# Kernel optimization log

Measured on AMD Instinct MI355X. Metric: run time of the kernel, lower is better.

Reference implementation:

```python
import jax, jax.numpy as jnp
import numpy as np

N, M, FIN, FOUT, K = 16, 65536, 32, 32, 7


def setup_inputs() -> dict:
    key = jax.random.key(0)
    k1, k2, k3, k4, k5 = jax.random.split(key, 5)
    stdv = 1.0 / np.sqrt(FIN)
    x = jax.random.normal(k1, (N, M, FIN), dtype=jnp.float32)
    weight = jax.random.uniform(k2, (K, FIN, FOUT), dtype=jnp.float32, minval=-stdv, maxval=stdv)
    bias = jax.random.uniform(k3, (FOUT,), dtype=jnp.float32, minval=-stdv, maxval=stdv)
    index_list = jax.random.randint(k4, (M * K,), 0, M, dtype=jnp.int32)
    index_value = jax.random.uniform(k5, (M, K), dtype=jnp.float32)
    return {"x": x, "weight": weight, "bias": bias,
            "index_list": index_list, "index_value": index_value}


def reference(x, weight, bias, index_list, index_value):
    # out[n,m,o] = sum_k sum_f index_value[m,k] * x[n, idx[m,k], f] * weight[k,f,o] + bias[o]
    n, m, fin = x.shape
    k = index_value.shape[1]
    idx = index_list.reshape(m, k)            # [M, K] neighbor ids
    gathered = x[:, idx, :]                    # [N, M, K, Fin] gather of neighbor feats
    weighted = gathered * index_value[None, :, :, None]  # apply adjacency weights
    out = jnp.einsum('nmkf,kfo->nmo', weighted, weight) + bias
    return out
```

## Files before the change

kernel.cpp:

```cpp
#include <hip/hip_runtime.h>
#include <hip/hip_bf16.h>

#define N_    16
#define M_    65536
#define FIN_  32
#define FOUT_ 32
#define K_    7

typedef __bf16 bf16x8 __attribute__((ext_vector_type(8)));
typedef float  f32x4  __attribute__((ext_vector_type(4)));

__global__ __launch_bounds__(256, 4)
void gfc_kernel(const float* __restrict__ x,
                const float* __restrict__ w,
                const float* __restrict__ bias,
                const int*   __restrict__ index_list,
                const float* __restrict__ index_value,
                float* __restrict__ out)
{
    const int lane  = threadIdx.x & 63;
    const int col   = lane & 15;
    const int kgrp  = lane >> 4;

    const int waves_per_block = blockDim.x >> 6;
    const int wave_id     = blockIdx.x * waves_per_block + (threadIdx.x >> 6);
    const int total_waves = gridDim.x * waves_per_block;

    bf16x8 bfrag[K_][2];
    #pragma unroll
    for (int k = 0; k < K_; ++k) {
        #pragma unroll
        for (int h = 0; h < 2; ++h) {
            const float* wp = w + (size_t)k * (FIN_ * FOUT_)
                                + (size_t)(kgrp * 8) * FOUT_ + h * 16 + col;
            bf16x8 b;
            #pragma unroll
            for (int j = 0; j < 8; ++j)
                b[j] = (__bf16)wp[j * FOUT_];
            bfrag[k][h] = b;
        }
    }
    const float b_lo = bias[col];
    const float b_hi = bias[16 + col];

    for (int m = wave_id; m < M_; m += total_waves) {
        f32x4 acc0 = {0.f, 0.f, 0.f, 0.f};
        f32x4 acc1 = {0.f, 0.f, 0.f, 0.f};

        #pragma unroll
        for (int k = 0; k < K_; ++k) {
            const int   m2  = index_list[m * K_ + k];
            const float ivk = index_value[m * K_ + k];

            const float* ap = x + ((size_t)col * M_ + (size_t)m2) * FIN_ + kgrp * 8;
            const float4 v0 = *(const float4*)(ap);
            const float4 v1 = *(const float4*)(ap + 4);

            const float av[8] = {v0.x, v0.y, v0.z, v0.w, v1.x, v1.y, v1.z, v1.w};
            bf16x8 a;
            #pragma unroll
            for (int j = 0; j < 8; ++j)
                a[j] = (__bf16)(av[j] * ivk);

            acc0 = __builtin_amdgcn_mfma_f32_16x16x32_bf16(a, bfrag[k][0], acc0, 0, 0, 0);
            acc1 = __builtin_amdgcn_mfma_f32_16x16x32_bf16(a, bfrag[k][1], acc1, 0, 0, 0);
        }

        #pragma unroll
        for (int r = 0; r < 4; ++r) {
            const int n = kgrp * 4 + r;
            const size_t base = ((size_t)n * M_ + (size_t)m) * FOUT_;
            out[base + col]      = acc0[r] + b_lo;
            out[base + 16 + col] = acc1[r] + b_hi;
        }
    }
}

extern "C" void kernel_launch(void* const* d_in, const int* in_sizes, int n_in,
                              void* d_out, int out_size, void* d_ws, size_t ws_size,
                              hipStream_t stream) {
    const float* x    = (const float*)d_in[0];
    const float* w    = (const float*)d_in[1];
    const float* bias = (const float*)d_in[2];
    const int*   il   = (const int*)  d_in[3];
    const float* iv   = (const float*)d_in[4];
    float* out = (float*)d_out;

    dim3 grid(2048), block(256);
    hipLaunchKernelGGL(gfc_kernel, grid, block, 0, stream, x, w, bias, il, iv, out);
}
```

Before: 363.5 us.

## Pre-transpose x to bf16 [M,N,F] layout for contiguous neighbor gathers

Adds a pre-pass that converts x to bf16 and lays it out as [M][N][FIN], so each gathered neighbor row of 16 batches by 32 features is one contiguous 1 KB block instead of 16 scattered 128-byte pieces. The main kernel loads all K indices and neighbor fragments up front to overlap memory latency, and uses readfirstlane to keep the row index scalar. The cost is an extra full pass over x (read fp32, write bf16) plus a workspace buffer. It also adds an extra rounding step, since x is rounded to bf16 before the index-value scale is applied. A fallback to the old kernel is kept for when the workspace is too small.

```diff
diff --git a/kernel.cpp b/kernel.cpp
--- a/kernel.cpp
+++ b/kernel.cpp
@@ -10,13 +10,108 @@
 typedef __bf16 bf16x8 __attribute__((ext_vector_type(8)));
 typedef float  f32x4  __attribute__((ext_vector_type(4)));
 
+__global__ __launch_bounds__(256)
+void transpose_kernel(const float* __restrict__ x, __bf16* __restrict__ xT)
+{
+    const int tid = blockIdx.x * blockDim.x + threadIdx.x;
+    const int f8 = tid & 3;
+    const int n  = (tid >> 2) & 15;
+    const int m  = tid >> 6;
+
+    const float4* src = (const float4*)(x + ((size_t)n * M_ + m) * FIN_ + f8 * 8);
+    const float4 v0 = src[0];
+    const float4 v1 = src[1];
+    const float av[8] = {v0.x, v0.y, v0.z, v0.w, v1.x, v1.y, v1.z, v1.w};
+
+    bf16x8 b;
+    #pragma unroll
+    for (int j = 0; j < 8; ++j) b[j] = (__bf16)av[j];
+
+    *(bf16x8*)(xT + ((size_t)m * N_ + n) * FIN_ + f8 * 8) = b;
+}
+
 __global__ __launch_bounds__(256, 4)
-void gfc_kernel(const float* __restrict__ x,
-                const float* __restrict__ w,
-                const float* __restrict__ bias,
-                const int*   __restrict__ index_list,
-                const float* __restrict__ index_value,
-                float* __restrict__ out)
+void gfc_bf16_kernel(const __bf16* __restrict__ xT,
+                     const float* __restrict__ w,
+                     const float* __restrict__ bias,
+                     const int*   __restrict__ index_list,
+                     const float* __restrict__ index_value,
+                     float* __restrict__ out)
+{
+    const int lane  = threadIdx.x & 63;
+    const int col   = lane & 15;
+    const int kgrp  = lane >> 4;
+
+    const int waves_per_block = blockDim.x >> 6;
+    const int wave_id     = blockIdx.x * waves_per_block + (threadIdx.x >> 6);
+    const int total_waves = gridDim.x * waves_per_block;
+
+    bf16x8 bfrag[K_][2];
+    #pragma unroll
+    for (int k = 0; k < K_; ++k) {
+        #pragma unroll
+        for (int h = 0; h < 2; ++h) {
+            const float* wp = w + (size_t)k * (FIN_ * FOUT_)
+                                + (size_t)(kgrp * 8) * FOUT_ + h * 16 + col;
+            bf16x8 b;
+            #pragma unroll
+            for (int j = 0; j < 8; ++j)
+                b[j] = (__bf16)wp[j * FOUT_];
+            bfrag[k][h] = b;
+        }
+    }
+    const float b_lo = bias[col];
+    const float b_hi = bias[16 + col];
+
+    const size_t lane_elt = (size_t)col * FIN_ + kgrp * 8;
+
+    for (int m0 = wave_id; m0 < M_; m0 += total_waves) {
+        const int m = __builtin_amdgcn_readfirstlane(m0);
+
+        f32x4 acc0 = {0.f, 0.f, 0.f, 0.f};
+        f32x4 acc1 = {0.f, 0.f, 0.f, 0.f};
+
+        int   idxs[K_];
+        float ivs[K_];
+        #pragma unroll
+        for (int k = 0; k < K_; ++k) {
+            idxs[k] = index_list[m * K_ + k];
+            ivs[k]  = index_value[m * K_ + k];
+        }
+
+        bf16x8 raw[K_];
+        #pragma unroll
+        for (int k = 0; k < K_; ++k)
+            raw[k] = *(const bf16x8*)(xT + (size_t)idxs[k] * (N_ * FIN_) + lane_elt);
+
+        #pragma unroll
+        for (int k = 0; k < K_; ++k) {
+            const float ivk = ivs[k];
+            bf16x8 a;
+            #pragma unroll
+            for (int j = 0; j < 8; ++j)
+                a[j] = (__bf16)((float)raw[k][j] * ivk);
+            acc0 = __builtin_amdgcn_mfma_f32_16x16x32_bf16(a, bfrag[k][0], acc0, 0, 0, 0);
+            acc1 = __builtin_amdgcn_mfma_f32_16x16x32_bf16(a, bfrag[k][1], acc1, 0, 0, 0);
+        }
+
+        #pragma unroll
+        for (int r = 0; r < 4; ++r) {
+            const int n = kgrp * 4 + r;
+            const size_t base = ((size_t)n * M_ + (size_t)m0) * FOUT_;
+            out[base + col]      = acc0[r] + b_lo;
+            out[base + 16 + col] = acc1[r] + b_hi;
+        }
+    }
+}
+
+__global__ __launch_bounds__(256, 4)
+void gfc_fallback_kernel(const float* __restrict__ x,
+                         const float* __restrict__ w,
+                         const float* __restrict__ bias,
+                         const int*   __restrict__ index_list,
+                         const float* __restrict__ index_value,
+                         float* __restrict__ out)
 {
     const int lane  = threadIdx.x & 63;
     const int col   = lane & 15;
@@ -51,17 +146,14 @@
         for (int k = 0; k < K_; ++k) {
             const int   m2  = index_list[m * K_ + k];
             const float ivk = index_value[m * K_ + k];
-
             const float* ap = x + ((size_t)col * M_ + (size_t)m2) * FIN_ + kgrp * 8;
             const float4 v0 = *(const float4*)(ap);
             const float4 v1 = *(const float4*)(ap + 4);
-
             const float av[8] = {v0.x, v0.y, v0.z, v0.w, v1.x, v1.y, v1.z, v1.w};
             bf16x8 a;
             #pragma unroll
             for (int j = 0; j < 8; ++j)
                 a[j] = (__bf16)(av[j] * ivk);
-
             acc0 = __builtin_amdgcn_mfma_f32_16x16x32_bf16(a, bfrag[k][0], acc0, 0, 0, 0);
             acc1 = __builtin_amdgcn_mfma_f32_16x16x32_bf16(a, bfrag[k][1], acc1, 0, 0, 0);
         }
@@ -86,6 +178,16 @@
     const float* iv   = (const float*)d_in[4];
     float* out = (float*)d_out;
 
-    dim3 grid(2048), block(256);
-    hipLaunchKernelGGL(gfc_kernel, grid, block, 0, stream, x, w, bias, il, iv, out);
+    const size_t ws_needed = (size_t)M_ * N_ * FIN_ * sizeof(__bf16);
+    if (ws_size >= ws_needed) {
+        __bf16* xT = (__bf16*)d_ws;
+        const int t_total  = N_ * M_ * FIN_ / 8;
+        hipLaunchKernelGGL(transpose_kernel, dim3(t_total / 256), dim3(256), 0, stream,
+                           x, xT);
+        hipLaunchKernelGGL(gfc_bf16_kernel, dim3(2048), dim3(256), 0, stream,
+                           xT, w, bias, il, iv, out);
+    } else {
+        hipLaunchKernelGGL(gfc_fallback_kernel, dim3(2048), dim3(256), 0, stream,
+                           x, w, bias, il, iv, out);
+    }
 }
```

New measurement: 314.5 us. -13.5%, faster.
